# Performance work log

Measured on AMD Instinct MI355X. Metric: run time of the kernel, lower is better.

The kernel has to match this reference:

```python
import jax, jax.numpy as jnp
import numpy as np

WIN = 7
K1 = 0.01
K2 = 0.03
NP_ = WIN * WIN
COV_NORM = NP_ / (NP_ - 1)


def _box(t):
    # 7x7 uniform box filter, VALID padding, NCHW layout
    w = jnp.ones((1, 1, WIN, WIN), t.dtype) / NP_
    return jax.lax.conv_general_dilated(
        t, w, window_strides=(1, 1), padding='VALID',
        dimension_numbers=('NCHW', 'OIHW', 'NCHW'))


def setup_inputs() -> dict:
    key = jax.random.key(0)
    kx, ky = jax.random.split(key)
    X = jax.random.normal(kx, (64, 512, 512), dtype=jnp.float32)
    Y = jax.random.normal(ky, (64, 512, 512), dtype=jnp.float32)
    return {"X": X, "Y": Y}


def reference(X, Y):
    # X: [B,H,W] -> [B,1,H,W]; Y: abs then channel dim (matches torch forward)
    Xc = X[:, None, :, :]
    Yc = jnp.abs(Y)[:, None, :, :]

    # data range per (B,C): max over spatial dims
    max_values = jnp.max(Yc, axis=(2, 3), keepdims=True)  # [B,1,1,1]
    C1 = (K1 * max_values) ** 2
    C2 = (K2 * max_values) ** 2

    ux = _box(Xc)
    uy = _box(Yc)
    uxx = _box(Xc * Xc)
    uyy = _box(Yc * Yc)
    uxy = _box(Xc * Yc)

    vx = COV_NORM * (uxx - ux * ux)
    vy = COV_NORM * (uyy - uy * uy)
    vxy = COV_NORM * (uxy - ux * uy)

    A1 = 2 * ux * uy + C1
    A2 = 2 * vxy + C2
    B1 = ux * ux + uy * uy + C1
    B2 = vx + vy + C2

    S = (A1 * A2) / (B1 * B2)
    return jnp.mean(1 - S)
```

## Files before the change

### kernel.cpp

```cpp
#include <hip/hip_runtime.h>

#define WIN 7
constexpr int H = 512, W = 512;
constexpr int OH = H - WIN + 1;
constexpr int OW = W - WIN + 1;
constexpr float INV_NP = 1.0f / 49.0f;
constexpr float COV_NORM = 49.0f / 48.0f;

#define TW 256
#define RT 32
#define SEGS 16

__global__ __launch_bounds__(256) void batch_max_kernel(const float* __restrict__ Y,
                                                        float* __restrict__ maxv,
                                                        float* __restrict__ out) {
    const int b   = blockIdx.x >> 4;
    const int seg = blockIdx.x & (SEGS - 1);
    constexpr int SEG_F4 = H * W / SEGS / 4;
    const float4* p = (const float4*)(Y + (size_t)b * H * W) + (size_t)seg * SEG_F4;
    float m = 0.f;
    #pragma unroll 4
    for (int i = threadIdx.x; i < SEG_F4; i += 256) {
        float4 v = p[i];
        m = fmaxf(m, fmaxf(fmaxf(fabsf(v.x), fabsf(v.y)),
                           fmaxf(fabsf(v.z), fabsf(v.w))));
    }
    #pragma unroll
    for (int off = 32; off > 0; off >>= 1)
        m = fmaxf(m, __shfl_down(m, off, 64));
    __shared__ float smax[4];
    const int wave = threadIdx.x >> 6;
    const int lane = threadIdx.x & 63;
    if (lane == 0) smax[wave] = m;
    __syncthreads();
    if (threadIdx.x == 0) {
        const float bm = fmaxf(fmaxf(smax[0], smax[1]), fmaxf(smax[2], smax[3]));
        atomicMax((int*)&maxv[b], __float_as_int(bm));
        if (blockIdx.x == 0) out[0] = 0.f;
    }
}

__global__ __launch_bounds__(256) void ssim_kernel(const float* __restrict__ X,
                                                   const float* __restrict__ Y,
                                                   const float* __restrict__ maxv,
                                                   float* __restrict__ out,
                                                   float inv_total) {
    const int b    = blockIdx.z;
    const int col0 = blockIdx.x * TW;
    const int r0   = blockIdx.y * RT;
    const int nr   = min(RT, OH - r0);
    const int nri  = nr + WIN - 1;
    const int ncols = min(TW + WIN - 1, W - col0);

    const float mv = maxv[b];
    const float C1 = (0.01f * mv) * (0.01f * mv);
    const float C2 = (0.03f * mv) * (0.03f * mv);

    const size_t base = (size_t)b * H * W;
    const float* Xb = X + base;
    const float* Yb = Y + base;

    __shared__ float2 lds[WIN][TW + WIN - 1];

    const int tid = threadIdx.x;
    const bool active = (col0 + tid) < OW;

    float ring_x[WIN], ring_y[WIN], ring_xx[WIN], ring_yy[WIN], ring_xy[WIN];
    #pragma unroll
    for (int k = 0; k < WIN; ++k) {
        ring_x[k] = 0.f; ring_y[k] = 0.f; ring_xx[k] = 0.f;
        ring_yy[k] = 0.f; ring_xy[k] = 0.f;
    }
    float vs_x = 0.f, vs_y = 0.f, vs_xx = 0.f, vs_yy = 0.f, vs_xy = 0.f;
    float acc = 0.f;

    for (int t = 0; t < nri; t += WIN) {
        const int nrows_chunk = min(WIN, nri - t);
        for (int r = 0; r < nrows_chunk; ++r) {
            const int gr = r0 + t + r;
            const float* xrow = Xb + (size_t)gr * W + col0;
            const float* yrow = Yb + (size_t)gr * W + col0;
            for (int c = tid; c < TW + WIN - 1; c += 256) {
                float xv = 0.f, yv = 0.f;
                if (c < ncols) { xv = xrow[c]; yv = fabsf(yrow[c]); }
                lds[r][c] = make_float2(xv, yv);
            }
        }
        __syncthreads();
        #pragma unroll
        for (int k = 0; k < WIN; ++k) {
            if (k < nrows_chunk) {
                const int tt = t + k;
                float hx = 0.f, hy = 0.f, hxx = 0.f, hyy = 0.f, hxy = 0.f;
                #pragma unroll
                for (int j = 0; j < WIN; ++j) {
                    float2 v = lds[k][tid + j];
                    hx += v.x;
                    hy += v.y;
                    hxx = fmaf(v.x, v.x, hxx);
                    hyy = fmaf(v.y, v.y, hyy);
                    hxy = fmaf(v.x, v.y, hxy);
                }
                vs_x  += hx  - ring_x[k];  ring_x[k]  = hx;
                vs_y  += hy  - ring_y[k];  ring_y[k]  = hy;
                vs_xx += hxx - ring_xx[k]; ring_xx[k] = hxx;
                vs_yy += hyy - ring_yy[k]; ring_yy[k] = hyy;
                vs_xy += hxy - ring_xy[k]; ring_xy[k] = hxy;
                if (tt >= WIN - 1 && active) {
                    const float ux  = vs_x  * INV_NP;
                    const float uy  = vs_y  * INV_NP;
                    const float uxx = vs_xx * INV_NP;
                    const float uyy = vs_yy * INV_NP;
                    const float uxy = vs_xy * INV_NP;
                    const float vx  = COV_NORM * (uxx - ux * ux);
                    const float vy  = COV_NORM * (uyy - uy * uy);
                    const float vxy = COV_NORM * (uxy - ux * uy);
                    const float A1 = 2.f * ux * uy + C1;
                    const float A2 = 2.f * vxy + C2;
                    const float B1 = ux * ux + uy * uy + C1;
                    const float B2 = vx + vy + C2;
                    const float S = (A1 * A2) * __builtin_amdgcn_rcpf(B1 * B2);
                    acc += 1.f - S;
                }
            }
        }
        __syncthreads();
    }

    acc *= inv_total;
    #pragma unroll
    for (int off = 32; off > 0; off >>= 1)
        acc += __shfl_down(acc, off, 64);
    __shared__ float sacc[4];
    const int wave = tid >> 6;
    const int lane = tid & 63;
    if (lane == 0) sacc[wave] = acc;
    __syncthreads();
    if (tid == 0)
        atomicAdd(out, sacc[0] + sacc[1] + sacc[2] + sacc[3]);
}

extern "C" void kernel_launch(void* const* d_in, const int* in_sizes, int n_in,
                              void* d_out, int out_size, void* d_ws, size_t ws_size,
                              hipStream_t stream) {
    const float* X = (const float*)d_in[0];
    const float* Y = (const float*)d_in[1];
    float* out  = (float*)d_out;
    float* maxv = (float*)d_ws;
    const int B = in_sizes[0] / (H * W);

    batch_max_kernel<<<B * SEGS, 256, 0, stream>>>(Y, maxv, out);

    dim3 grid((OW + TW - 1) / TW, (OH + RT - 1) / RT, B);
    const float inv_total = 1.0f / ((float)B * (float)OW * (float)OH);
    ssim_kernel<<<grid, 256, 0, stream>>>(X, Y, maxv, out, inv_total);
}
```

Baseline: 219.3 us.

## Give each wave its own column span with register row prefetch and no block barriers

Restructures the SSIM kernel so each 64-lane wave owns an independent 64-column span. Each wave stages one row at a time in a private LDS buffer and prefetches the next row's X/Y values into registers, which removes the block-wide __syncthreads between row chunks. Row tiles grow from 32 to 64 rows, so vertical halo reloads go down, but each wave now reloads its own 6-column halo and the grid has half as many blocks. Correctness of the LDS write-then-read relies on implicit wave lockstep, with no explicit wave barrier.

```diff
diff --git a/kernel.cpp b/kernel.cpp
--- a/kernel.cpp
+++ b/kernel.cpp
@@ -7,8 +7,6 @@
 constexpr float INV_NP = 1.0f / 49.0f;
 constexpr float COV_NORM = 49.0f / 48.0f;
 
-#define TW 256
-#define RT 32
 #define SEGS 16
 
 __global__ __launch_bounds__(256) void batch_max_kernel(const float* __restrict__ Y,
@@ -40,30 +38,34 @@
     }
 }
 
-__global__ __launch_bounds__(256) void ssim_kernel(const float* __restrict__ X,
-                                                   const float* __restrict__ Y,
-                                                   const float* __restrict__ maxv,
-                                                   float* __restrict__ out,
-                                                   float inv_total) {
+__global__ __launch_bounds__(256, 4) void ssim_kernel(const float* __restrict__ X,
+                                                      const float* __restrict__ Y,
+                                                      const float* __restrict__ maxv,
+                                                      float* __restrict__ out,
+                                                      float inv_total) {
+    const int wid  = threadIdx.x >> 6;
+    const int lane = threadIdx.x & 63;
+    const int span = blockIdx.x * 4 + wid;
+    const int col0 = span * 64;
+    const int r0   = blockIdx.y * 64;
     const int b    = blockIdx.z;
-    const int col0 = blockIdx.x * TW;
-    const int r0   = blockIdx.y * RT;
-    const int nr   = min(RT, OH - r0);
-    const int nri  = nr + WIN - 1;
-    const int ncols = min(TW + WIN - 1, W - col0);
+    const int nout = min(64, OH - r0);
+    const int nri  = nout + WIN - 1;
+    const bool active = (col0 + lane) < OW;
 
     const float mv = maxv[b];
     const float C1 = (0.01f * mv) * (0.01f * mv);
     const float C2 = (0.03f * mv) * (0.03f * mv);
 
+    __shared__ float2 rowbuf[4][72];
+    float2* rb = rowbuf[wid];
+
     const size_t base = (size_t)b * H * W;
-    const float* Xb = X + base;
-    const float* Yb = Y + base;
+    const int g1 = col0 + lane;
+    const bool t2 = (lane < 6) && (col0 + 64 + lane) < W;
 
-    __shared__ float2 lds[WIN][TW + WIN - 1];
-
-    const int tid = threadIdx.x;
-    const bool active = (col0 + tid) < OW;
+    const float* xp = X + base + (size_t)r0 * W + g1;
+    const float* yp = Y + base + (size_t)r0 * W + g1;
 
     float ring_x[WIN], ring_y[WIN], ring_xx[WIN], ring_yy[WIN], ring_xy[WIN];
     #pragma unroll
@@ -74,27 +76,28 @@
     float vs_x = 0.f, vs_y = 0.f, vs_xx = 0.f, vs_yy = 0.f, vs_xy = 0.f;
     float acc = 0.f;
 
+    float x1n = xp[0], y1n = yp[0];
+    float x2n = t2 ? xp[64] : 0.f, y2n = t2 ? yp[64] : 0.f;
+    xp += W; yp += W;
+
     for (int t = 0; t < nri; t += WIN) {
-        const int nrows_chunk = min(WIN, nri - t);
-        for (int r = 0; r < nrows_chunk; ++r) {
-            const int gr = r0 + t + r;
-            const float* xrow = Xb + (size_t)gr * W + col0;
-            const float* yrow = Yb + (size_t)gr * W + col0;
-            for (int c = tid; c < TW + WIN - 1; c += 256) {
-                float xv = 0.f, yv = 0.f;
-                if (c < ncols) { xv = xrow[c]; yv = fabsf(yrow[c]); }
-                lds[r][c] = make_float2(xv, yv);
-            }
-        }
-        __syncthreads();
         #pragma unroll
         for (int k = 0; k < WIN; ++k) {
-            if (k < nrows_chunk) {
-                const int tt = t + k;
+            const int i = t + k;
+            if (i < nri) {
+                rb[lane] = make_float2(x1n, fabsf(y1n));
+                if (lane < 6)
+                    rb[64 + lane] = t2 ? make_float2(x2n, fabsf(y2n))
+                                       : make_float2(0.f, 0.f);
+                if (i + 1 < nri) {
+                    x1n = xp[0]; y1n = yp[0];
+                    if (t2) { x2n = xp[64]; y2n = yp[64]; }
+                    xp += W; yp += W;
+                }
                 float hx = 0.f, hy = 0.f, hxx = 0.f, hyy = 0.f, hxy = 0.f;
                 #pragma unroll
                 for (int j = 0; j < WIN; ++j) {
-                    float2 v = lds[k][tid + j];
+                    float2 v = rb[lane + j];
                     hx += v.x;
                     hy += v.y;
                     hxx = fmaf(v.x, v.x, hxx);
@@ -106,7 +109,7 @@
                 vs_xx += hxx - ring_xx[k]; ring_xx[k] = hxx;
                 vs_yy += hyy - ring_yy[k]; ring_yy[k] = hyy;
                 vs_xy += hxy - ring_xy[k]; ring_xy[k] = hxy;
-                if (tt >= WIN - 1 && active) {
+                if (i >= WIN - 1 && active) {
                     const float ux  = vs_x  * INV_NP;
                     const float uy  = vs_y  * INV_NP;
                     const float uxx = vs_xx * INV_NP;
@@ -124,7 +127,6 @@
                 }
             }
         }
-        __syncthreads();
     }
 
     acc *= inv_total;
@@ -132,11 +134,9 @@
     for (int off = 32; off > 0; off >>= 1)
         acc += __shfl_down(acc, off, 64);
     __shared__ float sacc[4];
-    const int wave = tid >> 6;
-    const int lane = tid & 63;
-    if (lane == 0) sacc[wave] = acc;
+    if (lane == 0) sacc[wid] = acc;
     __syncthreads();
-    if (tid == 0)
+    if (threadIdx.x == 0)
         atomicAdd(out, sacc[0] + sacc[1] + sacc[2] + sacc[3]);
 }
 
@@ -151,7 +151,7 @@
 
     batch_max_kernel<<<B * SEGS, 256, 0, stream>>>(Y, maxv, out);
 
-    dim3 grid((OW + TW - 1) / TW, (OH + RT - 1) / RT, B);
+    dim3 grid(2, 8, B);
     const float inv_total = 1.0f / ((float)B * (float)OW * (float)OH);
     ssim_kernel<<<grid, 256, 0, stream>>>(X, Y, maxv, out, inv_total);
 }
```

Result: faster. 186.5 us (-15.0%).
